# Kernel optimization log

Hardware: AMD Instinct MI355X
Metric: run time of the kernel (lower is better)

## Reference

```python
import jax, jax.numpy as jnp
import numpy as np

BINS = 100
NORMALIZE = False
SIGMA = 1.0
B, N = 128, 512
EDGE_P = 0.02  # edge probability -> avg degree ~10


def _make_adj(key):
    u = jax.random.uniform(key, (B, N, N))
    a = (u < EDGE_P).astype(jnp.float32)
    up = jnp.triu(a, 1)
    return up + jnp.swapaxes(up, -1, -2)  # symmetric, zero diagonal


def setup_inputs() -> dict:
    key = jax.random.key(0)
    k1, k2 = jax.random.split(key)
    return {"adj_1": _make_adj(k1), "adj_2": _make_adj(k2)}


def _clustering_hist(adj):
    # adj: [B, N, N] binary symmetric, zero diag
    deg = adj.sum(-1)                                   # [B, N]
    a2 = jnp.matmul(adj, adj)                           # [B, N, N]
    tri2 = jnp.einsum('bij,bji->bi', a2, adj)           # diag(A^3) = 2 * triangles
    denom = deg * (deg - 1.0)
    # nx.clustering: c_i = 2*T_i / (k_i*(k_i-1)) = diag(A^3)_i / (k_i*(k_i-1)); 0 if k_i < 2
    c = jnp.where(denom > 0, tri2 / jnp.maximum(denom, 1.0), 0.0)  # [B, N] in [0,1]
    # histogram over [0,1] with BINS bins; value 1.0 falls in last bin (torch.histogram semantics)
    idx = jnp.clip((c * BINS).astype(jnp.int32), 0, BINS - 1)
    hist = jax.vmap(lambda ix: jnp.zeros((BINS,), jnp.float32).at[ix].add(1.0))(idx)
    if NORMALIZE:
        hist = hist * (BINS / N)  # density: count / (n_samples * bin_width)
    return hist  # [B, BINS]


def _rbf_mmd(x, y, sigma):
    # biased MMD^2 estimate with RBF kernel
    def kmat(a, b):
        sq = (a * a).sum(-1)[:, None] + (b * b).sum(-1)[None, :] - 2.0 * (a @ b.T)
        return jnp.exp(-jnp.maximum(sq, 0.0) / (2.0 * sigma * sigma))
    return kmat(x, x).mean() + kmat(y, y).mean() - 2.0 * kmat(x, y).mean()


def reference(adj_1, adj_2):
    h1 = _clustering_hist(adj_1)
    h2 = _clustering_hist(adj_2)
    return _rbf_mmd(h1, h2, SIGMA)
```

## Files before the change

kernel.cpp:

```cpp
#include <hip/hip_runtime.h>
#include <stdint.h>

#define BATCH 128
#define NN 512
#define BINS 100
#define WORDS 8
#define WPAD 9
#define ECAP 6144

__global__ __launch_bounds__(1024) void k_cluster_hist(
    const float* __restrict__ adj1, const float* __restrict__ adj2,
    float* __restrict__ hist )
{
    __shared__ unsigned long long bits[NN][WPAD];
    __shared__ unsigned int edges[ECAP];
    __shared__ int tri2[NN];
    __shared__ int histI[BINS];
    __shared__ int ecnt;

    const int gb = blockIdx.x;
    const float* __restrict__ g =
        (gb < BATCH ? adj1 : adj2) + (size_t)(gb & (BATCH - 1)) * NN * NN;

    const int tid  = threadIdx.x;
    const int lane = tid & 63;
    const int wave = tid >> 6;

    if (tid < BINS) histI[tid] = 0;
    if (tid < NN)   tri2[tid]  = 0;
    if (tid == 0)   ecnt = 0;

    for (int r0 = wave * 32; r0 < wave * 32 + 32; r0 += 8) {
        float4 v[16];
        #pragma unroll
        for (int i = 0; i < 8; ++i) {
            const float* rowp = g + (size_t)(r0 + i) * NN + 4 * lane;
            v[2 * i + 0] = *(const float4*)(rowp);
            v[2 * i + 1] = *(const float4*)(rowp + 256);
        }
        #pragma unroll
        for (int i = 0; i < 8; ++i) {
            #pragma unroll
            for (int s = 0; s < 2; ++s) {
                float4 q = v[2 * i + s];
                unsigned long long m0 = __ballot(q.x != 0.0f);
                unsigned long long m1 = __ballot(q.y != 0.0f);
                unsigned long long m2 = __ballot(q.z != 0.0f);
                unsigned long long m3 = __ballot(q.w != 0.0f);
                if (lane == 0) {
                    bits[r0 + i][s * 4 + 0] = m0;
                    bits[r0 + i][s * 4 + 1] = m1;
                    bits[r0 + i][s * 4 + 2] = m2;
                    bits[r0 + i][s * 4 + 3] = m3;
                }
            }
        }
    }
    __syncthreads();

    for (int p = tid; p < NN * WORDS; p += 1024) {
        int r = p >> 3;
        int m = p & 7;
        unsigned long long w = bits[r][m];
        int jbase = ((m >> 2) << 8) + (m & 3);
        unsigned long long wm = w;
        int d = r - jbase;
        if (d >= 0) {
            int Lmin = (d >> 2) + 1;
            wm = (Lmin >= 64) ? 0ull : (w & (~0ull << Lmin));
        }
        int cnt = __popcll(wm);

        int x = cnt;
        #pragma unroll
        for (int off = 1; off < 64; off <<= 1) {
            int y = __shfl_up(x, off, 64);
            if (lane >= off) x += y;
        }
        int excl = x - cnt;
        int base = 0;
        if (lane == 63) base = atomicAdd(&ecnt, x);
        base = __shfl(base, 63, 64);

        int idx = base + excl;
        while (wm) {
            int L = __builtin_ctzll(wm);
            wm &= wm - 1;
            int j = jbase + 4 * L;
            if (idx < ECAP) edges[idx] = ((unsigned)r << 10) | (unsigned)j;
            ++idx;
        }
    }
    __syncthreads();

    const int ne = ecnt < ECAP ? ecnt : ECAP;
    for (int e = tid; e < ne; e += 1024) {
        unsigned ed = edges[e];
        int i = ed >> 10;
        int j = ed & 1023;
        int acc = 0;
        #pragma unroll
        for (int w = 0; w < WORDS; ++w)
            acc += __popcll(bits[i][w] & bits[j][w]);
        atomicAdd(&tri2[i], acc);
        atomicAdd(&tri2[j], acc);
    }
    __syncthreads();

    if (tid < NN) {
        int deg = 0;
        #pragma unroll
        for (int w = 0; w < WORDS; ++w) deg += __popcll(bits[tid][w]);
        float t2    = (float)tri2[tid];
        float degf  = (float)deg;
        float denom = degf * (degf - 1.0f);
        float c = denom > 0.0f ? t2 / denom : 0.0f;
        int idx = (int)(c * 100.0f);
        idx = idx < 0 ? 0 : (idx > BINS - 1 ? BINS - 1 : idx);
        atomicAdd(&histI[idx], 1);
    }
    __syncthreads();

    if (tid < BINS) hist[(size_t)gb * BINS + tid] = (float)histI[tid];
}

__global__ __launch_bounds__(256) void k_mmd_partial(
    const float* __restrict__ hist, float* __restrict__ partials)
{
    int p = blockIdx.x * 256 + threadIdx.x;
    int t   = p >> 14;
    int rem = p & 16383;
    int i = rem >> 7;
    int j = rem & 127;
    const float4* x4;
    const float4* y4;
    float w;
    if (t == 0)      { x4 = (const float4*)(hist + (size_t)i * BINS);           y4 = (const float4*)(hist + (size_t)j * BINS);           w =  1.0f; }
    else if (t == 1) { x4 = (const float4*)(hist + (size_t)(BATCH + i) * BINS); y4 = (const float4*)(hist + (size_t)(BATCH + j) * BINS); w =  1.0f; }
    else             { x4 = (const float4*)(hist + (size_t)i * BINS);           y4 = (const float4*)(hist + (size_t)(BATCH + j) * BINS); w = -2.0f; }
    float sq = 0.0f;
    #pragma unroll
    for (int k = 0; k < BINS / 4; ++k) {
        float4 a = x4[k];
        float4 b = y4[k];
        float d0 = a.x - b.x, d1 = a.y - b.y, d2 = a.z - b.z, d3 = a.w - b.w;
        sq += d0 * d0 + d1 * d1 + d2 * d2 + d3 * d3;
    }
    float local = w * expf(-0.5f * sq);

    __shared__ float red[256];
    red[threadIdx.x] = local;
    __syncthreads();
    for (int s = 128; s >= 1; s >>= 1) {
        if (threadIdx.x < s) red[threadIdx.x] += red[threadIdx.x + s];
        __syncthreads();
    }
    if (threadIdx.x == 0) partials[blockIdx.x] = red[0];
}

__global__ __launch_bounds__(64) void k_mmd_final(
    const float* __restrict__ partials, float* __restrict__ out, int nparts)
{
    int lane = threadIdx.x;
    float v = 0.0f;
    for (int p = lane; p < nparts; p += 64) v += partials[p];
    #pragma unroll
    for (int off = 32; off >= 1; off >>= 1) v += __shfl_xor(v, off, 64);
    if (lane == 0) out[0] = v * (1.0f / (float)(BATCH * BATCH));
}

extern "C" void kernel_launch(void* const* d_in, const int* in_sizes, int n_in,
                              void* d_out, int out_size, void* d_ws, size_t ws_size,
                              hipStream_t stream) {
    const float* a1 = (const float*)d_in[0];
    const float* a2 = (const float*)d_in[1];
    float* hist     = (float*)d_ws;
    float* partials = (float*)((char*)d_ws + 2 * BATCH * BINS * sizeof(float));
    float* out      = (float*)d_out;

    hipLaunchKernelGGL(k_cluster_hist, dim3(2 * BATCH), dim3(1024), 0, stream,
                       a1, a2, hist);
    hipLaunchKernelGGL(k_mmd_partial, dim3(192), dim3(256), 0, stream,
                       hist, partials);
    hipLaunchKernelGGL(k_mmd_final, dim3(1), dim3(64), 0, stream,
                       partials, out, 192);
}
```

Baseline: 290.0 us.

## Split adjacency bit-packing into a separate high-occupancy grid-wide kernel

Moves the float-to-bitmask packing of the adjacency matrices out of the per-graph 1024-thread kernel into a separate kernel with 2048 blocks of 256 threads. The packed bits go to workspace, and a second kernel loads them into shared memory and does the triangle counting and histogram. The aim is to spread the 268MB read across more waves and CUs instead of 256 large blocks limited by shared memory. In exchange it adds an extra launch and a global round trip for the 2MB of packed bits, and it falls back to the old path when the workspace is too small.

```diff
diff --git a/kernel.cpp b/kernel.cpp
--- a/kernel.cpp
+++ b/kernel.cpp
@@ -7,10 +7,148 @@
 #define WORDS 8
 #define WPAD 9
 #define ECAP 6144
+#define PACK_BLOCKS 2048
+
+
+__global__ __launch_bounds__(256) void k_pack(
+    const float* __restrict__ adj1, const float* __restrict__ adj2,
+    unsigned long long* __restrict__ bits_g )
+{
+    const int lane = threadIdx.x & 63;
+    const int wid  = blockIdx.x * (blockDim.x >> 6) + (threadIdx.x >> 6);
+    const int nw   = gridDim.x * (blockDim.x >> 6);
+    const int NUNIT = 2 * BATCH * NN * 2;
+
+    for (int u0 = wid * 4; u0 < NUNIT; u0 += nw * 4) {
+        float4 v[4];
+        #pragma unroll
+        for (int k = 0; k < 4; ++k) {
+            int u  = u0 + k;
+            int gb = u >> 10;
+            int ui = u & 1023;
+            int r  = ui >> 1;
+            int sg = ui & 1;
+            const float* p = (gb < BATCH ? adj1 : adj2)
+                           + (size_t)(gb & (BATCH - 1)) * NN * NN
+                           + (size_t)r * NN + sg * 256 + 4 * lane;
+            v[k] = *(const float4*)p;
+        }
+        #pragma unroll
+        for (int k = 0; k < 4; ++k) {
+            int u  = u0 + k;
+            int gb = u >> 10;
+            int ui = u & 1023;
+            int r  = ui >> 1;
+            int sg = ui & 1;
+            unsigned long long m0 = __ballot(v[k].x != 0.0f);
+            unsigned long long m1 = __ballot(v[k].y != 0.0f);
+            unsigned long long m2 = __ballot(v[k].z != 0.0f);
+            unsigned long long m3 = __ballot(v[k].w != 0.0f);
+            unsigned long long* dst =
+                bits_g + ((size_t)(gb * NN + r) * WORDS) + sg * 4;
+            unsigned long long lo = lane ? m2 : m0;
+            unsigned long long hi = lane ? m3 : m1;
+            if (lane < 2) {
+                ulonglong2 w; w.x = lo; w.y = hi;
+                *(ulonglong2*)(dst + 2 * lane) = w;
+            }
+        }
+    }
+}
+
+__global__ __launch_bounds__(1024) void k_tri_hist(
+    const unsigned long long* __restrict__ bits_g,
+    float* __restrict__ hist )
+{
+    __shared__ unsigned long long bits[NN][WPAD];
+    __shared__ unsigned int edges[ECAP];
+    __shared__ int tri2[NN];
+    __shared__ int histI[BINS];
+    __shared__ int ecnt;
+
+    const int gb  = blockIdx.x;
+    const int tid = threadIdx.x;
+    const int lane = tid & 63;
+    const unsigned long long* src = bits_g + (size_t)gb * NN * WORDS;
+
+    if (tid < BINS) histI[tid] = 0;
+    if (tid < NN)   tri2[tid]  = 0;
+    if (tid == 0)   ecnt = 0;
+
+    #pragma unroll
+    for (int g = tid; g < NN * WORDS; g += 1024)
+        bits[g >> 3][g & 7] = src[g];
+    __syncthreads();
+
+    for (int p = tid; p < NN * WORDS; p += 1024) {
+        int r = p >> 3;
+        int m = p & 7;
+        unsigned long long w = bits[r][m];
+        int jbase = ((m >> 2) << 8) + (m & 3);
+        unsigned long long wm = w;
+        int d = r - jbase;
+        if (d >= 0) {
+            int Lmin = (d >> 2) + 1;
+            wm = (Lmin >= 64) ? 0ull : (w & (~0ull << Lmin));
+        }
+        int cnt = __popcll(wm);
+
+        int x = cnt;
+        #pragma unroll
+        for (int off = 1; off < 64; off <<= 1) {
+            int y = __shfl_up(x, off, 64);
+            if (lane >= off) x += y;
+        }
+        int excl = x - cnt;
+        int base = 0;
+        if (lane == 63) base = atomicAdd(&ecnt, x);
+        base = __shfl(base, 63, 64);
+
+        int idx = base + excl;
+        while (wm) {
+            int L = __builtin_ctzll(wm);
+            wm &= wm - 1;
+            int j = jbase + 4 * L;
+            if (idx < ECAP) edges[idx] = ((unsigned)r << 10) | (unsigned)j;
+            ++idx;
+        }
+    }
+    __syncthreads();
+
+    const int ne = ecnt < ECAP ? ecnt : ECAP;
+    for (int e = tid; e < ne; e += 1024) {
+        unsigned ed = edges[e];
+        int i = ed >> 10;
+        int j = ed & 1023;
+        int acc = 0;
+        #pragma unroll
+        for (int w = 0; w < WORDS; ++w)
+            acc += __popcll(bits[i][w] & bits[j][w]);
+        atomicAdd(&tri2[i], acc);
+        atomicAdd(&tri2[j], acc);
+    }
+    __syncthreads();
+
+    if (tid < NN) {
+        int deg = 0;
+        #pragma unroll
+        for (int w = 0; w < WORDS; ++w) deg += __popcll(bits[tid][w]);
+        float t2    = (float)tri2[tid];
+        float degf  = (float)deg;
+        float denom = degf * (degf - 1.0f);
+        float c = denom > 0.0f ? t2 / denom : 0.0f;
+        int idx = (int)(c * 100.0f);
+        idx = idx < 0 ? 0 : (idx > BINS - 1 ? BINS - 1 : idx);
+        atomicAdd(&histI[idx], 1);
+    }
+    __syncthreads();
+
+    if (tid < BINS) hist[(size_t)gb * BINS + tid] = (float)histI[tid];
+}
 
 __global__ __launch_bounds__(1024) void k_cluster_hist(
     const float* __restrict__ adj1, const float* __restrict__ adj2,
-    float* __restrict__ hist )
+    float* __restrict__ hist)
 {
     __shared__ unsigned long long bits[NN][WPAD];
     __shared__ unsigned int edges[ECAP];
@@ -70,7 +208,6 @@
             wm = (Lmin >= 64) ? 0ull : (w & (~0ull << Lmin));
         }
         int cnt = __popcll(wm);
-
         int x = cnt;
         #pragma unroll
         for (int off = 1; off < 64; off <<= 1) {
@@ -81,7 +218,6 @@
         int base = 0;
         if (lane == 63) base = atomicAdd(&ecnt, x);
         base = __shfl(base, 63, 64);
-
         int idx = base + excl;
         while (wm) {
             int L = __builtin_ctzll(wm);
@@ -174,14 +310,32 @@
                               hipStream_t stream) {
     const float* a1 = (const float*)d_in[0];
     const float* a2 = (const float*)d_in[1];
-    float* hist     = (float*)d_ws;
-    float* partials = (float*)((char*)d_ws + 2 * BATCH * BINS * sizeof(float));
-    float* out      = (float*)d_out;
-
-    hipLaunchKernelGGL(k_cluster_hist, dim3(2 * BATCH), dim3(1024), 0, stream,
-                       a1, a2, hist);
-    hipLaunchKernelGGL(k_mmd_partial, dim3(192), dim3(256), 0, stream,
-                       hist, partials);
-    hipLaunchKernelGGL(k_mmd_final, dim3(1), dim3(64), 0, stream,
-                       partials, out, 192);
-}
+    float* out = (float*)d_out;
+
+    const size_t bits_bytes = (size_t)2 * BATCH * NN * WORDS * 8;
+    const size_t hist_bytes = (size_t)2 * BATCH * BINS * 4;
+    const size_t need = bits_bytes + hist_bytes + 192 * 4;
+
+    if (ws_size >= need) {
+        unsigned long long* bits_g = (unsigned long long*)d_ws;
+        float* hist     = (float*)((char*)d_ws + bits_bytes);
+        float* partials = (float*)((char*)d_ws + bits_bytes + hist_bytes);
+        hipLaunchKernelGGL(k_pack, dim3(PACK_BLOCKS), dim3(256), 0, stream,
+                           a1, a2, bits_g);
+        hipLaunchKernelGGL(k_tri_hist, dim3(2 * BATCH), dim3(1024), 0, stream,
+                           bits_g, hist);
+        hipLaunchKernelGGL(k_mmd_partial, dim3(192), dim3(256), 0, stream,
+                           hist, partials);
+        hipLaunchKernelGGL(k_mmd_final, dim3(1), dim3(64), 0, stream,
+                           partials, out, 192);
+    } else {
+        float* hist     = (float*)d_ws;
+        float* partials = (float*)((char*)d_ws + hist_bytes);
+        hipLaunchKernelGGL(k_cluster_hist, dim3(2 * BATCH), dim3(1024), 0, stream,
+                           a1, a2, hist);
+        hipLaunchKernelGGL(k_mmd_partial, dim3(192), dim3(256), 0, stream,
+                           hist, partials);
+        hipLaunchKernelGGL(k_mmd_final, dim3(1), dim3(64), 0, stream,
+                           partials, out, 192);
+    }
+}
```

Result: no change. 288.5 us (-0.5%).

## Split adjacency bit-packing into separate wide-grid kernel before triangle counting

Applied to the files above, without the earlier changes.

Moves the float-to-bitmask packing of the adjacency matrices out of the 256-block triangle kernel into its own kernel with 2048 blocks. Each lane packs 32 contiguous columns into a 32-bit word, so the bitmask layout becomes natural column order and the edge extraction math simplifies. The aim is to spread the dominant 268MB streaming read over many more waves and improve memory-level parallelism. The cost is an extra launch and a global round trip of the packed bits, about 2MB.

```diff
diff --git a/kernel.cpp b/kernel.cpp
--- a/kernel.cpp
+++ b/kernel.cpp
@@ -7,9 +7,45 @@
 #define WORDS 8
 #define WPAD 9
 #define ECAP 6144
-
-__global__ __launch_bounds__(1024) void k_cluster_hist(
+#define PACK_BLOCKS 2048
+
+__global__ __launch_bounds__(256) void k_pack(
     const float* __restrict__ adj1, const float* __restrict__ adj2,
+    unsigned int* __restrict__ bits32 )
+{
+    const int lane = threadIdx.x & 63;
+    const int wid  = blockIdx.x * 4 + (threadIdx.x >> 6);
+    const int gb   = wid >> 5;
+    const int lw   = wid & 31;
+    const float* __restrict__ gp =
+        (gb < BATCH ? adj1 : adj2) + (size_t)(gb & (BATCH - 1)) * NN * NN;
+    const int rsub = lane >> 4;
+    const int cw   = lane & 15;
+
+    for (int u = lw; u < NN / 4; u += 32) {
+        int r = 4 * u + rsub;
+        const float4* __restrict__ p4 =
+            (const float4*)(gp + (size_t)r * NN + cw * 32);
+        float4 f[8];
+        #pragma unroll
+        for (int k = 0; k < 8; ++k) f[k] = p4[k];
+#if __has_builtin(__builtin_amdgcn_sched_barrier)
+        __builtin_amdgcn_sched_barrier(0);
+#endif
+        unsigned m = 0u;
+        #pragma unroll
+        for (int k = 0; k < 8; ++k) {
+            m |= (f[k].x != 0.0f ? 1u : 0u) << (4 * k + 0);
+            m |= (f[k].y != 0.0f ? 1u : 0u) << (4 * k + 1);
+            m |= (f[k].z != 0.0f ? 1u : 0u) << (4 * k + 2);
+            m |= (f[k].w != 0.0f ? 1u : 0u) << (4 * k + 3);
+        }
+        bits32[((size_t)gb * NN + r) * 16 + cw] = m;
+    }
+}
+
+__global__ __launch_bounds__(1024) void k_tri_hist(
+    const unsigned long long* __restrict__ bits_g,
     float* __restrict__ hist )
 {
     __shared__ unsigned long long bits[NN][WPAD];
@@ -18,57 +54,28 @@
     __shared__ int histI[BINS];
     __shared__ int ecnt;
 
-    const int gb = blockIdx.x;
-    const float* __restrict__ g =
-        (gb < BATCH ? adj1 : adj2) + (size_t)(gb & (BATCH - 1)) * NN * NN;
-
-    const int tid  = threadIdx.x;
+    const int gb  = blockIdx.x;
+    const int tid = threadIdx.x;
     const int lane = tid & 63;
-    const int wave = tid >> 6;
+    const unsigned long long* src = bits_g + (size_t)gb * NN * WORDS;
 
     if (tid < BINS) histI[tid] = 0;
     if (tid < NN)   tri2[tid]  = 0;
     if (tid == 0)   ecnt = 0;
 
-    for (int r0 = wave * 32; r0 < wave * 32 + 32; r0 += 8) {
-        float4 v[16];
-        #pragma unroll
-        for (int i = 0; i < 8; ++i) {
-            const float* rowp = g + (size_t)(r0 + i) * NN + 4 * lane;
-            v[2 * i + 0] = *(const float4*)(rowp);
-            v[2 * i + 1] = *(const float4*)(rowp + 256);
-        }
-        #pragma unroll
-        for (int i = 0; i < 8; ++i) {
-            #pragma unroll
-            for (int s = 0; s < 2; ++s) {
-                float4 q = v[2 * i + s];
-                unsigned long long m0 = __ballot(q.x != 0.0f);
-                unsigned long long m1 = __ballot(q.y != 0.0f);
-                unsigned long long m2 = __ballot(q.z != 0.0f);
-                unsigned long long m3 = __ballot(q.w != 0.0f);
-                if (lane == 0) {
-                    bits[r0 + i][s * 4 + 0] = m0;
-                    bits[r0 + i][s * 4 + 1] = m1;
-                    bits[r0 + i][s * 4 + 2] = m2;
-                    bits[r0 + i][s * 4 + 3] = m3;
-                }
-            }
-        }
-    }
+    #pragma unroll
+    for (int g = tid; g < NN * WORDS; g += 1024)
+        bits[g >> 3][g & 7] = src[g];
     __syncthreads();
 
     for (int p = tid; p < NN * WORDS; p += 1024) {
         int r = p >> 3;
         int m = p & 7;
         unsigned long long w = bits[r][m];
-        int jbase = ((m >> 2) << 8) + (m & 3);
-        unsigned long long wm = w;
-        int d = r - jbase;
-        if (d >= 0) {
-            int Lmin = (d >> 2) + 1;
-            wm = (Lmin >= 64) ? 0ull : (w & (~0ull << Lmin));
-        }
+        int base = m << 6;
+        int sh = r - base + 1;
+        unsigned long long wm =
+            (sh <= 0) ? w : (sh >= 64 ? 0ull : (w & (~0ull << sh)));
         int cnt = __popcll(wm);
 
         int x = cnt;
@@ -78,15 +85,15 @@
             if (lane >= off) x += y;
         }
         int excl = x - cnt;
-        int base = 0;
-        if (lane == 63) base = atomicAdd(&ecnt, x);
-        base = __shfl(base, 63, 64);
-
-        int idx = base + excl;
+        int bs = 0;
+        if (lane == 63) bs = atomicAdd(&ecnt, x);
+        bs = __shfl(bs, 63, 64);
+
+        int idx = bs + excl;
         while (wm) {
             int L = __builtin_ctzll(wm);
             wm &= wm - 1;
-            int j = jbase + 4 * L;
+            int j = base + L;
             if (idx < ECAP) edges[idx] = ((unsigned)r << 10) | (unsigned)j;
             ++idx;
         }
@@ -174,12 +181,19 @@
                               hipStream_t stream) {
     const float* a1 = (const float*)d_in[0];
     const float* a2 = (const float*)d_in[1];
-    float* hist     = (float*)d_ws;
-    float* partials = (float*)((char*)d_ws + 2 * BATCH * BINS * sizeof(float));
-    float* out      = (float*)d_out;
-
-    hipLaunchKernelGGL(k_cluster_hist, dim3(2 * BATCH), dim3(1024), 0, stream,
-                       a1, a2, hist);
+    float* out = (float*)d_out;
+
+    const size_t bits_bytes = (size_t)2 * BATCH * NN * WORDS * 8;
+    const size_t hist_bytes = (size_t)2 * BATCH * BINS * 4;
+
+    unsigned int* bits32 = (unsigned int*)d_ws;
+    float* hist     = (float*)((char*)d_ws + bits_bytes);
+    float* partials = (float*)((char*)d_ws + bits_bytes + hist_bytes);
+
+    hipLaunchKernelGGL(k_pack, dim3(PACK_BLOCKS), dim3(256), 0, stream,
+                       a1, a2, bits32);
+    hipLaunchKernelGGL(k_tri_hist, dim3(2 * BATCH), dim3(1024), 0, stream,
+                       (const unsigned long long*)bits32, hist);
     hipLaunchKernelGGL(k_mmd_partial, dim3(192), dim3(256), 0, stream,
                        hist, partials);
     hipLaunchKernelGGL(k_mmd_final, dim3(1), dim3(64), 0, stream,
```

Result: no change. 293.4 us (+1.1%).

## Read only upper-triangle adjacency blocks and rebuild lower half by bit transpose

Applied to the files above, without the earlier changes.

Uses the symmetry of the adjacency matrix. Each row now loads only the 64-column blocks on or above the diagonal, which roughly halves the global reads of the dense float input. The lower-triangular 64x64 bit blocks are then rebuilt with a wave-level shuffle-based bit-matrix transpose. The bit layout changes from interleaved columns to contiguous columns, so edge extraction is updated to match. In exchange it adds spread/transpose ALU work and relies on the input being exactly symmetric.

```diff
diff --git a/kernel.cpp b/kernel.cpp
--- a/kernel.cpp
+++ b/kernel.cpp
@@ -7,6 +7,14 @@
 #define WORDS 8
 #define WPAD 9
 #define ECAP 6144
+
+__device__ __forceinline__ unsigned long long spread4(unsigned long long x) {
+    x = (x | (x << 24)) & 0x000000ff000000ffull;
+    x = (x | (x << 12)) & 0x000f000f000f000full;
+    x = (x | (x <<  6)) & 0x0303030303030303ull;
+    x = (x | (x <<  3)) & 0x1111111111111111ull;
+    return x;
+}
 
 __global__ __launch_bounds__(1024) void k_cluster_hist(
     const float* __restrict__ adj1, const float* __restrict__ adj2,
@@ -19,7 +27,7 @@
     __shared__ int ecnt;
 
     const int gb = blockIdx.x;
-    const float* __restrict__ g =
+    const float* __restrict__ gp =
         (gb < BATCH ? adj1 : adj2) + (size_t)(gb & (BATCH - 1)) * NN * NN;
 
     const int tid  = threadIdx.x;
@@ -30,31 +38,46 @@
     if (tid < NN)   tri2[tid]  = 0;
     if (tid == 0)   ecnt = 0;
 
-    for (int r0 = wave * 32; r0 < wave * 32 + 32; r0 += 8) {
-        float4 v[16];
-        #pragma unroll
-        for (int i = 0; i < 8; ++i) {
-            const float* rowp = g + (size_t)(r0 + i) * NN + 4 * lane;
-            v[2 * i + 0] = *(const float4*)(rowp);
-            v[2 * i + 1] = *(const float4*)(rowp + 256);
-        }
-        #pragma unroll
-        for (int i = 0; i < 8; ++i) {
-            #pragma unroll
-            for (int s = 0; s < 2; ++s) {
-                float4 q = v[2 * i + s];
-                unsigned long long m0 = __ballot(q.x != 0.0f);
-                unsigned long long m1 = __ballot(q.y != 0.0f);
-                unsigned long long m2 = __ballot(q.z != 0.0f);
-                unsigned long long m3 = __ballot(q.w != 0.0f);
-                if (lane == 0) {
-                    bits[r0 + i][s * 4 + 0] = m0;
-                    bits[r0 + i][s * 4 + 1] = m1;
-                    bits[r0 + i][s * 4 + 2] = m2;
-                    bits[r0 + i][s * 4 + 3] = m3;
-                }
-            }
-        }
+    for (int r = wave; r < NN; r += 16) {
+        const int br = r >> 6;
+        const int nb = 8 - br;
+        const int c0 = br << 6;
+        float4 v = make_float4(0.f, 0.f, 0.f, 0.f);
+        if (lane < 16 * nb)
+            v = *(const float4*)(gp + (size_t)r * NN + c0 + 4 * lane);
+        unsigned long long b0 = __ballot(v.x != 0.0f);
+        unsigned long long b1 = __ballot(v.y != 0.0f);
+        unsigned long long b2 = __ballot(v.z != 0.0f);
+        unsigned long long b3 = __ballot(v.w != 0.0f);
+        if (lane < nb) {
+            const int sh = 16 * lane;
+            unsigned long long w =
+                (spread4((b0 >> sh) & 0xFFFFull) << 0) |
+                (spread4((b1 >> sh) & 0xFFFFull) << 1) |
+                (spread4((b2 >> sh) & 0xFFFFull) << 2) |
+                (spread4((b3 >> sh) & 0xFFFFull) << 3);
+            bits[r][br + lane] = w;
+        }
+    }
+    __syncthreads();
+
+    for (int p = wave; p < 28; p += 16) {
+        int bi = 1;
+        while (bi * (bi + 1) / 2 <= p) ++bi;
+        const int bj = p - bi * (bi - 1) / 2;
+        unsigned long long x = bits[(bj << 6) + lane][bi];
+        const unsigned long long M[6] = {
+            0x5555555555555555ull, 0x3333333333333333ull,
+            0x0f0f0f0f0f0f0f0full, 0x00ff00ff00ff00ffull,
+            0x0000ffff0000ffffull, 0x00000000ffffffffull };
+        #pragma unroll
+        for (int s = 0; s < 6; ++s) {
+            const int k = 1 << s;
+            unsigned long long y = __shfl_xor((long long)x, k, 64);
+            if ((lane & k) == 0) x = (x &  M[s]) | ((y &  M[s]) << k);
+            else                 x = (x & ~M[s]) | ((y & ~M[s]) >> k);
+        }
+        bits[(bi << 6) + lane][bj] = x;
     }
     __syncthreads();
 
@@ -62,13 +85,10 @@
         int r = p >> 3;
         int m = p & 7;
         unsigned long long w = bits[r][m];
-        int jbase = ((m >> 2) << 8) + (m & 3);
-        unsigned long long wm = w;
-        int d = r - jbase;
-        if (d >= 0) {
-            int Lmin = (d >> 2) + 1;
-            wm = (Lmin >= 64) ? 0ull : (w & (~0ull << Lmin));
-        }
+        int base = m << 6;
+        int sh = r - base + 1;
+        unsigned long long wm =
+            (sh <= 0) ? w : (sh >= 64 ? 0ull : (w & (~0ull << sh)));
         int cnt = __popcll(wm);
 
         int x = cnt;
@@ -78,15 +98,15 @@
             if (lane >= off) x += y;
         }
         int excl = x - cnt;
-        int base = 0;
-        if (lane == 63) base = atomicAdd(&ecnt, x);
-        base = __shfl(base, 63, 64);
-
-        int idx = base + excl;
+        int bs = 0;
+        if (lane == 63) bs = atomicAdd(&ecnt, x);
+        bs = __shfl(bs, 63, 64);
+
+        int idx = bs + excl;
         while (wm) {
             int L = __builtin_ctzll(wm);
             wm &= wm - 1;
-            int j = jbase + 4 * L;
+            int j = base + L;
             if (idx < ECAP) edges[idx] = ((unsigned)r << 10) | (unsigned)j;
             ++idx;
         }
@@ -174,9 +194,11 @@
                               hipStream_t stream) {
     const float* a1 = (const float*)d_in[0];
     const float* a2 = (const float*)d_in[1];
+    float* out = (float*)d_out;
+
+    const size_t hist_bytes = (size_t)2 * BATCH * BINS * 4;
     float* hist     = (float*)d_ws;
-    float* partials = (float*)((char*)d_ws + 2 * BATCH * BINS * sizeof(float));
-    float* out      = (float*)d_out;
+    float* partials = (float*)((char*)d_ws + hist_bytes);
 
     hipLaunchKernelGGL(k_cluster_hist, dim3(2 * BATCH), dim3(1024), 0, stream,
                        a1, a2, hist);
```

New measurement: 255.9 us. -11.8%, faster.
